# Optimization experiments

Hardware: AMD Instinct MI355X
Metric: run time of the kernel (lower is better)

The kernel has to match this reference:

```python
import jax, jax.numpy as jnp
import numpy as np

T, B, F = 128, 128, 1024
ALPHA_BASE, LAMBDA_BASE = 0.97, 0.95
THETA_BASE, BETA_THETA = 0.1, 0.01
RHO, GATE_ALPHA = 0.25, 5.0        # gate_cfg rho_B/rho_C, alpha
NUDGE, PHASE_SCALE = 0.1, 0.02     # gate_cfg additive_nudge, ei_cfg phase_corr_scale
MIX_AMP, MIX_NOV, MIX_INST = 1.0, 0.5, 0.5


def _adaptive_percentile_threshold(score, rho, alpha):
    # keep top-rho fraction per row: tau = (1-rho)-quantile, soft sigmoid gate
    tau = jnp.quantile(score, 1.0 - rho, axis=-1, keepdims=True)
    return jax.nn.sigmoid(alpha * (score - tau)), tau


def setup_inputs() -> dict:
    key = jax.random.key(0)
    k0, k1, k2, k3 = jax.random.split(key, 4)
    return {
        "in_re": jax.random.normal(k0, (T, B, F), jnp.float32),
        "in_im": jax.random.normal(k1, (T, B, F), jnp.float32),
        "r_re": 0.05 * jax.random.normal(k2, (F,), jnp.float32),
        "r_im": 0.05 * jax.random.normal(k3, (F,), jnp.float32),
        "alpha_map": jnp.zeros((F,), jnp.float32),
        "lambda_map": jnp.zeros((F,), jnp.float32),
    }


def reference(in_re, in_im, r_re, r_im, alpha_map, lambda_map):
    sg = jax.lax.stop_gradient
    alpha = jnp.clip(ALPHA_BASE + 0.05 * jnp.tanh(alpha_map), 0.9, 0.995)  # [F]
    lam = jnp.clip(LAMBDA_BASE + 0.05 * jnp.tanh(lambda_map), 0.9, 0.995)  # [F]
    r_conj = jnp.conj(r_re + 1j * r_im)                                    # [F] c64
    theta_base = jnp.full((F,), THETA_BASE, jnp.float32)
    in_field = (in_re + 1j * in_im).astype(jnp.complex64)                  # [T,B,F]

    carry0 = dict(
        X=jnp.zeros((B, F), jnp.complex64),
        sA=jnp.zeros((B, F), jnp.float32),
        sB=jnp.zeros((B, F), jnp.float32),
        sC=jnp.zeros((B, F), jnp.float32),
        theta=theta_base,
        mu=jnp.zeros((F,), jnp.float32),
        var=jnp.full((F,), 0.01, jnp.float32),
        ema_unit=jnp.zeros((F,), jnp.complex64),
        b_usage=jnp.zeros((F,), jnp.float32),
        c_usage=jnp.zeros((F,), jnp.float32),
    )

    def step(c, u):
        X_mid = alpha * c["X"] + u                       # [B,F] c64
        amp = jnp.abs(X_mid)
        unit = jnp.exp(1j * jnp.angle(X_mid))            # unit phase
        # EMA stats (torch.no_grad -> stop_gradient)
        mu = sg(0.9 * c["mu"] + 0.1 * amp.mean(0))
        var = sg(0.9 * c["var"] + 0.1 * ((amp - mu[None]) ** 2).mean(0))
        ema_unit = sg(0.9 * c["ema_unit"] + 0.1 * unit.mean(0))
        plv = jnp.abs(ema_unit)                          # [F]
        zscore = (amp - mu[None]) / (jnp.sqrt(var)[None] + 1e-3)
        instab = (1.0 - plv)[None]
        score = MIX_AMP * amp + MIX_NOV * jnp.abs(zscore) + MIX_INST * instab
        gB, _ = _adaptive_percentile_threshold(score, RHO, GATE_ALPHA)
        gC, _ = _adaptive_percentile_threshold(-score, RHO, GATE_ALPHA)
        XB = X_mid * gB
        XC = X_mid * gC
        sA = lam * c["sA"] + jnp.real(X_mid * r_conj)
        sB = lam * c["sB"] + jnp.real(XB * r_conj)
        sC = lam * c["sC"] + jnp.real(XC * r_conj)
        evA = (sA >= c["theta"]).astype(jnp.float32)
        evB = (sB >= c["theta"]).astype(jnp.float32)
        evC = (sC >= c["theta"]).astype(jnp.float32)
        # threshold homeostasis (no_grad)
        theta = c["theta"] + 0.01 * evB.mean(0) - 0.01 * evC.mean(0)
        theta = jnp.clip(theta - BETA_THETA * (theta - theta_base), 0.01, 10.0)
        # reentry_mode='full': phase correction + additive nudge
        corr = (evB.mean(0) > 0).astype(jnp.float32)[None]  # [1,F]
        XA = X_mid * jnp.exp(1j * PHASE_SCALE * corr)
        XA = XA + NUDGE * (XB * corr)
        b_usage = 0.99 * c["b_usage"] + 0.01 * evB.mean(0)
        c_usage = 0.99 * c["c_usage"] + 0.01 * evC.mean(0)
        new = dict(X=XA, sA=sA, sB=sB, sC=sC, theta=theta, mu=mu, var=var,
                   ema_unit=ema_unit, b_usage=b_usage, c_usage=c_usage)
        return new, sA

    _, sA_seq = jax.lax.scan(step, carry0, in_field)
    return sA_seq  # [T,B,F]
```

## Files before the change

### kernel.cpp

```cpp
#include <hip/hip_runtime.h>
#include <math.h>


#define T_STEPS 128
#define B_DIM   128
#define F_DIM   1024
#define NWG     128
#define NTH     1024
#define BF      (B_DIM * F_DIM)

typedef unsigned long long ull;

__device__ __forceinline__ ull ld64(const ull* p) {
  return __hip_atomic_load(p, __ATOMIC_RELAXED, __HIP_MEMORY_SCOPE_AGENT);
}
__device__ __forceinline__ void st64(ull* p, ull v) {
  __hip_atomic_store(p, v, __ATOMIC_RELAXED, __HIP_MEMORY_SCOPE_AGENT);
}

extern "C" __global__ void __launch_bounds__(NTH)
ResonatorABC_82094004896068_kernel(
    const float* __restrict__ in_re, const float* __restrict__ in_im,
    const float* __restrict__ r_re_p, const float* __restrict__ r_im_p,
    const float* __restrict__ alpha_map, const float* __restrict__ lambda_map,
    float* __restrict__ out, ull* __restrict__ ws)
{
  const int tid  = threadIdx.x;
  const int wg   = blockIdx.x;
  const int b    = tid >> 3;
  const int fl   = tid & 7;
  const int f    = (wg << 3) + fl;
  const int wid  = tid >> 6;
  const int lane = tid & 63;
  const int idx  = b * F_DIM + f;

  ull* score64 = ws;
  ull* tauB64  = ws + BF;
  ull* tauC64  = ws + BF + 128;

  __shared__ __align__(16) float pamp[16][8][4];
  __shared__ __align__(16) float pfin[8][4];
  __shared__ __align__(16) float pev[16][8][2];
  __shared__ __align__(16) float evfin[8][2];
  __shared__ unsigned h[1024];
  __shared__ unsigned wsum[16];
  __shared__ unsigned mmw[16][2];
  __shared__ unsigned mmu[2];
  __shared__ unsigned tbin[4], tbase[4], tcnt[4];
  __shared__ unsigned lcnt[4];
  __shared__ unsigned lists[4][256];
  __shared__ unsigned resv[4], resf[4];
  __shared__ unsigned rmm[2];
  __shared__ unsigned t2[3];
  __shared__ float tauLds[256];

  float af = fminf(fmaxf(0.97f + 0.05f * tanhf(alpha_map[f]), 0.90f), 0.995f);
  float lf = fminf(fmaxf(0.95f + 0.05f * tanhf(lambda_map[f]), 0.90f), 0.995f);
  float rr = r_re_p[f];
  float ri = r_im_p[f];
  const float c002 = cosf(0.02f);
  const float s002 = sinf(0.02f);

  float X_re = 0.f, X_im = 0.f, sA = 0.f, sB = 0.f, sC = 0.f;
  float mu = 0.f, var = 0.01f, theta = 0.1f, ema_re = 0.f, ema_im = 0.f;

  float ur = in_re[idx];
  float ui = in_im[idx];

  const unsigned KR0 = 255u, KR1 = 256u, KR2 = 767u, KR3 = 768u;

  for (int t = 0; t < T_STEPS; ++t) {
    const ull want = (ull)(t + 1);

    h[tid] = 0u;

    float Xm_re = af * X_re + ur;
    float Xm_im = af * X_im + ui;
    float amp2 = Xm_re * Xm_re + Xm_im * Xm_im;
    float amp  = sqrtf(amp2);
    float invamp = (amp > 0.f) ? (1.0f / amp) : 0.f;
    float un_re = (amp > 0.f) ? (Xm_re * invamp) : 1.0f;
    float un_im = Xm_im * invamp;
    float proj = Xm_re * rr + Xm_im * ri;
    sA = lf * sA + proj;
    out[t * BF + idx] = sA;

    float r0 = amp, r1 = amp2, r2 = un_re, r3 = un_im;
    #pragma unroll
    for (int m = 8; m < 64; m <<= 1) {
      r0 += __shfl_xor(r0, m);
      r1 += __shfl_xor(r1, m);
      r2 += __shfl_xor(r2, m);
      r3 += __shfl_xor(r3, m);
    }
    if (lane < 8) { *(float4*)&pamp[wid][lane][0] = make_float4(r0, r1, r2, r3); }
    __syncthreads();
    if (tid < 32) {
      int sfl = tid >> 2, q = tid & 3;
      float s = 0.f;
      #pragma unroll
      for (int w = 0; w < 16; ++w) s += pamp[w][sfl][q];
      pfin[sfl][q] = s;
    }
    __syncthreads();
    float4 SS = *(const float4*)&pfin[fl][0];
    float m1 = SS.x * 0.0078125f;
    float m2 = SS.y * 0.0078125f;
    mu = 0.9f * mu + 0.1f * m1;
    float vm = m2 - 2.f * mu * m1 + mu * mu;
    vm = fmaxf(vm, 0.f);
    var = 0.9f * var + 0.1f * vm;
    ema_re = 0.9f * ema_re + 0.1f * (SS.z * 0.0078125f);
    ema_im = 0.9f * ema_im + 0.1f * (SS.w * 0.0078125f);
    float plv = sqrtf(ema_re * ema_re + ema_im * ema_im);
    float zs = (amp - mu) / (sqrtf(var) + 1e-3f);
    float score = amp + 0.5f * fabsf(zs) + 0.5f * (1.0f - plv);
    st64(&score64[idx], (want << 32) | (ull)__float_as_uint(score));

    float ur_n = 0.f, ui_n = 0.f;
    if (t + 1 < T_STEPS) {
      ur_n = in_re[(t + 1) * BF + idx];
      ui_n = in_im[(t + 1) * BF + idx];
    }

    const ull* spoll = &score64[wg * F_DIM + tid];
    ull v = ld64(spoll);
    while ((v >> 32) != want) { __builtin_amdgcn_s_sleep(1); v = ld64(spoll); }
    unsigned uval = (unsigned)v;

    unsigned umin = uval, umax = uval;
    #pragma unroll
    for (int m = 1; m < 64; m <<= 1) {
      umin = min(umin, (unsigned)__shfl_xor((int)umin, m));
      umax = max(umax, (unsigned)__shfl_xor((int)umax, m));
    }
    if (lane == 0) { mmw[wid][0] = umin; mmw[wid][1] = umax; }
    __syncthreads();
    if (tid < 16) {
      unsigned a = mmw[tid][0], c = mmw[tid][1];
      #pragma unroll
      for (int m = 1; m < 16; m <<= 1) {
        a = min(a, (unsigned)__shfl_xor((int)a, m));
        c = max(c, (unsigned)__shfl_xor((int)c, m));
      }
      if (tid == 0) { mmu[0] = a; mmu[1] = c; }
    }
    __syncthreads();
    unsigned lo = mmu[0], hi = mmu[1];

    if (lo != hi) {
      ull rng = (ull)hi - (ull)lo + 1ull;
      ull inv = (1ull << 40) / rng;
      unsigned bin = (unsigned)((((ull)(uval - lo)) * inv) >> 30);
      atomicAdd(&h[bin], 1u);
      __syncthreads();
      unsigned cnt = h[tid];
      unsigned incl = cnt;
      #pragma unroll
      for (int d = 1; d < 64; d <<= 1) {
        unsigned vv = __shfl_up(incl, d);
        if (lane >= d) incl += vv;
      }
      if (lane == 63) wsum[wid] = incl;
      __syncthreads();
      if (tid < 16) {
        unsigned wv = wsum[tid], wincl = wv;
        #pragma unroll
        for (int d = 1; d < 16; d <<= 1) {
          unsigned x = __shfl_up(wincl, d);
          if (tid >= d) wincl += x;
        }
        wsum[tid] = wincl - wv;
      }
      if (tid < 4) { lcnt[tid] = 0u; resf[tid] = 0u; }
      __syncthreads();
      unsigned base = wsum[wid] + (incl - cnt);
      if (cnt > 0u) {
        if (base <= KR0 && KR0 < base + cnt) { tbin[0] = tid; tbase[0] = base; tcnt[0] = cnt; }
        if (base <= KR1 && KR1 < base + cnt) { tbin[1] = tid; tbase[1] = base; tcnt[1] = cnt; }
        if (base <= KR2 && KR2 < base + cnt) { tbin[2] = tid; tbase[2] = base; tcnt[2] = cnt; }
        if (base <= KR3 && KR3 < base + cnt) { tbin[3] = tid; tbase[3] = base; tcnt[3] = cnt; }
      }
      __syncthreads();
      unsigned b0 = tbin[0], b1 = tbin[1], b2 = tbin[2], b3 = tbin[3];
      if (bin == b0) { unsigned s = atomicAdd(&lcnt[0], 1u); if (s < 256u) lists[0][s] = uval; }
      else if (bin == b1 && b1 != b0) { unsigned s = atomicAdd(&lcnt[1], 1u); if (s < 256u) lists[1][s] = uval; }
      else if (bin == b2 && b2 != b1) { unsigned s = atomicAdd(&lcnt[2], 1u); if (s < 256u) lists[2][s] = uval; }
      else if (bin == b3 && b3 != b2) { unsigned s = atomicAdd(&lcnt[3], 1u); if (s < 256u) lists[3][s] = uval; }
      __syncthreads();
      if (wid < 4) {
        const int j = wid;
        const unsigned KRj = (j == 0) ? KR0 : (j == 1) ? KR1 : (j == 2) ? KR2 : KR3;
        int src = j;
        while (src > 0 && tbin[src - 1] == tbin[j]) --src;
        unsigned c = tcnt[j];
        if (c <= 256u) {
          unsigned kk = KRj - tbase[j];
          for (int bi = 0; bi < (int)c; bi += 64) {
            int i = bi + lane;
            if (i < (int)c) {
              unsigned e = lists[src][i];
              unsigned r = 0;
              for (int q = 0; q < (int)c; ++q) {
                unsigned x = lists[src][q];
                r += (x < e || (x == e && q < i)) ? 1u : 0u;
              }
              if (r == kk) { resv[j] = e; resf[j] = 1u; }
            }
          }
        }
      }
      __syncthreads();
      for (int j = 0; j < 4; ++j) {
        if (resf[j]) continue;
        const unsigned KRj = (j == 0) ? KR0 : (j == 1) ? KR1 : (j == 2) ? KR2 : KR3;
        bool inj = (bin == tbin[j]);
        unsigned krem = KRj - tbase[j];
        for (int iter = 0; iter < 40; ++iter) {
          if (tid == 0) { rmm[0] = 0xFFFFFFFFu; rmm[1] = 0u; }
          __syncthreads();
          if (inj) { atomicMin(&rmm[0], uval); atomicMax(&rmm[1], uval); }
          __syncthreads();
          unsigned wlo = rmm[0], whi = rmm[1];
          if (wlo == whi) { if (tid == 0) { resv[j] = wlo; resf[j] = 1u; } __syncthreads(); break; }
          h[tid] = 0u;
          __syncthreads();
          ull rng2 = (ull)whi - (ull)wlo + 1ull;
          ull inv2 = (1ull << 40) / rng2;
          unsigned nb = inj ? (unsigned)((((ull)(uval - wlo)) * inv2) >> 30) : 0u;
          if (inj) atomicAdd(&h[nb], 1u);
          __syncthreads();
          unsigned cnt2 = h[tid];
          unsigned incl2 = cnt2;
          #pragma unroll
          for (int d = 1; d < 64; d <<= 1) {
            unsigned vv = __shfl_up(incl2, d);
            if (lane >= d) incl2 += vv;
          }
          if (lane == 63) wsum[wid] = incl2;
          __syncthreads();
          if (tid < 16) {
            unsigned wv = wsum[tid], wincl = wv;
            #pragma unroll
            for (int d = 1; d < 16; d <<= 1) {
              unsigned x = __shfl_up(wincl, d);
              if (tid >= d) wincl += x;
            }
            wsum[tid] = wincl - wv;
          }
          if (tid == 0) lcnt[0] = 0u;
          __syncthreads();
          unsigned base2 = wsum[wid] + (incl2 - cnt2);
          if (cnt2 > 0u && base2 <= krem && krem < base2 + cnt2) {
            t2[0] = tid; t2[1] = base2; t2[2] = cnt2;
          }
          __syncthreads();
          unsigned nbin = t2[0], nbase = t2[1], ncnt = t2[2];
          bool newin = inj && (nb == nbin);
          if (ncnt <= 256u) {
            if (newin) { unsigned s = atomicAdd(&lcnt[0], 1u); if (s < 256u) lists[0][s] = uval; }
            __syncthreads();
            if (wid == 0) {
              unsigned kk2 = krem - nbase;
              for (int bi = 0; bi < (int)ncnt; bi += 64) {
                int i = bi + lane;
                if (i < (int)ncnt) {
                  unsigned e = lists[0][i];
                  unsigned r = 0;
                  for (int q = 0; q < (int)ncnt; ++q) {
                    unsigned x = lists[0][q];
                    r += (x < e || (x == e && q < i)) ? 1u : 0u;
                  }
                  if (r == kk2) { resv[j] = e; resf[j] = 1u; }
                }
              }
            }
            __syncthreads();
            break;
          }
          inj = newin; krem = krem - nbase;
        }
      }
    } else {
      if (tid < 4) { resv[tid] = lo; resf[tid] = 1u; }
      __syncthreads();
    }
    if (tid == 0) {
      float s255 = __uint_as_float(resv[0]);
      float s256 = __uint_as_float(resv[1]);
      float s767 = __uint_as_float(resv[2]);
      float s768 = __uint_as_float(resv[3]);
      float tb = 0.75f * s767 + 0.25f * s768;
      float tc = -(0.75f * s256 + 0.25f * s255);
      st64(&tauB64[wg], (want << 32) | (ull)__float_as_uint(tb));
      st64(&tauC64[wg], (want << 32) | (ull)__float_as_uint(tc));
    }

    if (tid < 256) {
      const ull* src = (tid < 128) ? &tauB64[tid] : &tauC64[tid - 128];
      ull v2 = ld64(src);
      while ((v2 >> 32) != want) { __builtin_amdgcn_s_sleep(1); v2 = ld64(src); }
      tauLds[tid] = __uint_as_float((unsigned)v2);
    }
    __syncthreads();
    float tb = tauLds[b];
    float tc = tauLds[128 + b];

    float gB = 1.0f / (1.0f + expf(-5.0f * (score - tb)));
    float gC = 1.0f / (1.0f + expf(-5.0f * (-score - tc)));
    sB = lf * sB + proj * gB;
    sC = lf * sC + proj * gC;
    float e0 = (sB >= theta) ? 1.0f : 0.0f;
    float e1 = (sC >= theta) ? 1.0f : 0.0f;
    #pragma unroll
    for (int m = 8; m < 64; m <<= 1) {
      e0 += __shfl_xor(e0, m);
      e1 += __shfl_xor(e1, m);
    }
    if (lane < 8) { pev[wid][lane][0] = e0; pev[wid][lane][1] = e1; }
    __syncthreads();
    if (tid < 16) {
      int sfl = tid >> 1, q = tid & 1;
      float s = 0.f;
      #pragma unroll
      for (int w = 0; w < 16; ++w) s += pev[w][sfl][q];
      evfin[sfl][q] = s;
    }
    __syncthreads();
    float cB = evfin[fl][0];
    float cC = evfin[fl][1];
    float th1 = theta + 0.01f * (cB * 0.0078125f) - 0.01f * (cC * 0.0078125f);
    theta = fminf(fmaxf(th1 - 0.01f * (th1 - 0.1f), 0.01f), 10.0f);
    float fac_re = 1.0f, fac_im = 0.0f;
    if (cB > 0.f) { fac_re = c002 + 0.1f * gB; fac_im = s002; }
    X_re = Xm_re * fac_re - Xm_im * fac_im;
    X_im = Xm_re * fac_im + Xm_im * fac_re;

    ur = ur_n; ui = ui_n;
  }
}

extern "C" void kernel_launch(void* const* d_in, const int* in_sizes, int n_in,
                              void* d_out, int out_size, void* d_ws, size_t ws_size,
                              hipStream_t stream) {
  const float* in_re = (const float*)d_in[0];
  const float* in_im = (const float*)d_in[1];
  const float* r_re  = (const float*)d_in[2];
  const float* r_im  = (const float*)d_in[3];
  const float* amap  = (const float*)d_in[4];
  const float* lmap  = (const float*)d_in[5];
  float* out = (float*)d_out;
  ull* ws = (ull*)d_ws;
  hipMemsetAsync(d_ws, 0, (size_t)(BF + 256) * 8, stream);
  hipLaunchKernelGGL(ResonatorABC_82094004896068_kernel,
                     dim3(NWG), dim3(NTH), 0, stream,
                     in_re, in_im, r_re, r_im, amap, lmap, out, ws);
}
```

Measured before the change: 1.255 ms.

## Shrink workgroup to 256 threads, each handling four batch rows

Cuts the workgroup from 1024 threads to 256, with each thread handling four batch rows (b = rg + 32k) for the same feature column. Histogram, scan, min/max and event reductions are restructured to work on four elements per thread, with 4-wave cross-wave combines replacing 16-wave ones and one barrier round dropped. The aim is lower barrier and cross-wave reduction cost in this latency-bound, barrier-heavy per-timestep loop. The trade-off is more serial work per thread and more registers, which may lengthen the per-step critical path.

After: 1.208 ms. 1.04x faster.

```diff
diff --git a/kernel.cpp b/kernel.cpp
--- a/kernel.cpp
+++ b/kernel.cpp
@@ -6,7 +6,7 @@
 #define B_DIM   128
 #define F_DIM   1024
 #define NWG     128
-#define NTH     1024
+#define NTH     256
 #define BF      (B_DIM * F_DIM)
 
 typedef unsigned long long ull;
@@ -27,25 +27,23 @@
 {
   const int tid  = threadIdx.x;
   const int wg   = blockIdx.x;
-  const int b    = tid >> 3;
   const int fl   = tid & 7;
+  const int rg   = tid >> 3;
   const int f    = (wg << 3) + fl;
   const int wid  = tid >> 6;
   const int lane = tid & 63;
-  const int idx  = b * F_DIM + f;
 
   ull* score64 = ws;
   ull* tauB64  = ws + BF;
   ull* tauC64  = ws + BF + 128;
 
-  __shared__ __align__(16) float pamp[16][8][4];
+  __shared__ __align__(16) float pamp[4][8][4];
   __shared__ __align__(16) float pfin[8][4];
-  __shared__ __align__(16) float pev[16][8][2];
+  __shared__ __align__(16) float pev[4][8][2];
   __shared__ __align__(16) float evfin[8][2];
-  __shared__ unsigned h[1024];
-  __shared__ unsigned wsum[16];
-  __shared__ unsigned mmw[16][2];
-  __shared__ unsigned mmu[2];
+  __shared__ __align__(16) unsigned h[1024];
+  __shared__ unsigned wsum[4];
+  __shared__ unsigned mmw[4][2];
   __shared__ unsigned tbin[4], tbase[4], tcnt[4];
   __shared__ unsigned lcnt[4];
   __shared__ unsigned lists[4][256];
@@ -54,53 +52,61 @@
   __shared__ unsigned t2[3];
   __shared__ float tauLds[256];
 
-  float af = fminf(fmaxf(0.97f + 0.05f * tanhf(alpha_map[f]), 0.90f), 0.995f);
-  float lf = fminf(fmaxf(0.95f + 0.05f * tanhf(lambda_map[f]), 0.90f), 0.995f);
-  float rr = r_re_p[f];
-  float ri = r_im_p[f];
+  const float af = fminf(fmaxf(0.97f + 0.05f * tanhf(alpha_map[f]), 0.90f), 0.995f);
+  const float lf = fminf(fmaxf(0.95f + 0.05f * tanhf(lambda_map[f]), 0.90f), 0.995f);
+  const float rr = r_re_p[f];
+  const float ri = r_im_p[f];
   const float c002 = cosf(0.02f);
   const float s002 = sinf(0.02f);
 
-  float X_re = 0.f, X_im = 0.f, sA = 0.f, sB = 0.f, sC = 0.f;
+  float X_re[4] = {0.f,0.f,0.f,0.f}, X_im[4] = {0.f,0.f,0.f,0.f};
+  float sA[4] = {0.f,0.f,0.f,0.f}, sB[4] = {0.f,0.f,0.f,0.f}, sC[4] = {0.f,0.f,0.f,0.f};
   float mu = 0.f, var = 0.01f, theta = 0.1f, ema_re = 0.f, ema_im = 0.f;
 
-  float ur = in_re[idx];
-  float ui = in_im[idx];
-
-  const unsigned KR0 = 255u, KR1 = 256u, KR2 = 767u, KR3 = 768u;
+  int idx[4];
+  float ur[4], ui[4];
+  #pragma unroll
+  for (int k = 0; k < 4; ++k) {
+    idx[k] = (rg + 32 * k) * F_DIM + f;
+    ur[k] = in_re[idx[k]];
+    ui[k] = in_im[idx[k]];
+  }
+
+  const unsigned KR[4] = {255u, 256u, 767u, 768u};
 
   for (int t = 0; t < T_STEPS; ++t) {
     const ull want = (ull)(t + 1);
 
-    h[tid] = 0u;
-
-    float Xm_re = af * X_re + ur;
-    float Xm_im = af * X_im + ui;
-    float amp2 = Xm_re * Xm_re + Xm_im * Xm_im;
-    float amp  = sqrtf(amp2);
-    float invamp = (amp > 0.f) ? (1.0f / amp) : 0.f;
-    float un_re = (amp > 0.f) ? (Xm_re * invamp) : 1.0f;
-    float un_im = Xm_im * invamp;
-    float proj = Xm_re * rr + Xm_im * ri;
-    sA = lf * sA + proj;
-    out[t * BF + idx] = sA;
-
-    float r0 = amp, r1 = amp2, r2 = un_re, r3 = un_im;
+    *(uint4*)&h[4 * tid] = make_uint4(0u, 0u, 0u, 0u);
+
+    float Xm_re[4], Xm_im[4], proj[4], amp[4], score[4];
+    float a0 = 0.f, a1 = 0.f, a2 = 0.f, a3 = 0.f;
+    #pragma unroll
+    for (int k = 0; k < 4; ++k) {
+      Xm_re[k] = af * X_re[k] + ur[k];
+      Xm_im[k] = af * X_im[k] + ui[k];
+      float amp2 = Xm_re[k] * Xm_re[k] + Xm_im[k] * Xm_im[k];
+      amp[k] = sqrtf(amp2);
+      float invamp = (amp[k] > 0.f) ? (1.0f / amp[k]) : 0.f;
+      float un_re = (amp[k] > 0.f) ? (Xm_re[k] * invamp) : 1.0f;
+      float un_im = Xm_im[k] * invamp;
+      proj[k] = Xm_re[k] * rr + Xm_im[k] * ri;
+      sA[k] = lf * sA[k] + proj[k];
+      out[t * BF + idx[k]] = sA[k];
+      a0 += amp[k]; a1 += amp2; a2 += un_re; a3 += un_im;
+    }
     #pragma unroll
     for (int m = 8; m < 64; m <<= 1) {
-      r0 += __shfl_xor(r0, m);
-      r1 += __shfl_xor(r1, m);
-      r2 += __shfl_xor(r2, m);
-      r3 += __shfl_xor(r3, m);
-    }
-    if (lane < 8) { *(float4*)&pamp[wid][lane][0] = make_float4(r0, r1, r2, r3); }
+      a0 += __shfl_xor(a0, m);
+      a1 += __shfl_xor(a1, m);
+      a2 += __shfl_xor(a2, m);
+      a3 += __shfl_xor(a3, m);
+    }
+    if (lane < 8) { *(float4*)&pamp[wid][lane][0] = make_float4(a0, a1, a2, a3); }
     __syncthreads();
     if (tid < 32) {
       int sfl = tid >> 2, q = tid & 3;
-      float s = 0.f;
-      #pragma unroll
-      for (int w = 0; w < 16; ++w) s += pamp[w][sfl][q];
-      pfin[sfl][q] = s;
+      pfin[sfl][q] = pamp[0][sfl][q] + pamp[1][sfl][q] + pamp[2][sfl][q] + pamp[3][sfl][q];
     }
     __syncthreads();
     float4 SS = *(const float4*)&pfin[fl][0];
@@ -113,22 +119,35 @@
     ema_re = 0.9f * ema_re + 0.1f * (SS.z * 0.0078125f);
     ema_im = 0.9f * ema_im + 0.1f * (SS.w * 0.0078125f);
     float plv = sqrtf(ema_re * ema_re + ema_im * ema_im);
-    float zs = (amp - mu) / (sqrtf(var) + 1e-3f);
-    float score = amp + 0.5f * fabsf(zs) + 0.5f * (1.0f - plv);
-    st64(&score64[idx], (want << 32) | (ull)__float_as_uint(score));
-
-    float ur_n = 0.f, ui_n = 0.f;
+    float sden = sqrtf(var) + 1e-3f;
+    #pragma unroll
+    for (int k = 0; k < 4; ++k) {
+      float zs = (amp[k] - mu) / sden;
+      score[k] = amp[k] + 0.5f * fabsf(zs) + 0.5f * (1.0f - plv);
+      st64(&score64[idx[k]], (want << 32) | (ull)__float_as_uint(score[k]));
+    }
+
+    float ur_n[4] = {0.f,0.f,0.f,0.f}, ui_n[4] = {0.f,0.f,0.f,0.f};
     if (t + 1 < T_STEPS) {
-      ur_n = in_re[(t + 1) * BF + idx];
-      ui_n = in_im[(t + 1) * BF + idx];
-    }
-
-    const ull* spoll = &score64[wg * F_DIM + tid];
-    ull v = ld64(spoll);
-    while ((v >> 32) != want) { __builtin_amdgcn_s_sleep(1); v = ld64(spoll); }
-    unsigned uval = (unsigned)v;
-
-    unsigned umin = uval, umax = uval;
+      #pragma unroll
+      for (int k = 0; k < 4; ++k) {
+        ur_n[k] = in_re[(t + 1) * BF + idx[k]];
+        ui_n[k] = in_im[(t + 1) * BF + idx[k]];
+      }
+    }
+
+    unsigned uval[4], bin[4];
+    {
+      const ull* sp0 = &score64[wg * F_DIM + tid];
+      #pragma unroll
+      for (int k = 0; k < 4; ++k) {
+        ull v = ld64(sp0 + 256 * k);
+        while ((v >> 32) != want) { __builtin_amdgcn_s_sleep(1); v = ld64(sp0 + 256 * k); }
+        uval[k] = (unsigned)v;
+      }
+    }
+    unsigned umin = min(min(uval[0], uval[1]), min(uval[2], uval[3]));
+    unsigned umax = max(max(uval[0], uval[1]), max(uval[2], uval[3]));
     #pragma unroll
     for (int m = 1; m < 64; m <<= 1) {
       umin = min(umin, (unsigned)__shfl_xor((int)umin, m));
@@ -136,26 +155,22 @@
     }
     if (lane == 0) { mmw[wid][0] = umin; mmw[wid][1] = umax; }
     __syncthreads();
-    if (tid < 16) {
-      unsigned a = mmw[tid][0], c = mmw[tid][1];
-      #pragma unroll
-      for (int m = 1; m < 16; m <<= 1) {
-        a = min(a, (unsigned)__shfl_xor((int)a, m));
-        c = max(c, (unsigned)__shfl_xor((int)c, m));
-      }
-      if (tid == 0) { mmu[0] = a; mmu[1] = c; }
-    }
-    __syncthreads();
-    unsigned lo = mmu[0], hi = mmu[1];
+    unsigned lo = min(min(mmw[0][0], mmw[1][0]), min(mmw[2][0], mmw[3][0]));
+    unsigned hi = max(max(mmw[0][1], mmw[1][1]), max(mmw[2][1], mmw[3][1]));
 
     if (lo != hi) {
       ull rng = (ull)hi - (ull)lo + 1ull;
       ull inv = (1ull << 40) / rng;
-      unsigned bin = (unsigned)((((ull)(uval - lo)) * inv) >> 30);
-      atomicAdd(&h[bin], 1u);
-      __syncthreads();
-      unsigned cnt = h[tid];
-      unsigned incl = cnt;
+      #pragma unroll
+      for (int k = 0; k < 4; ++k) {
+        bin[k] = (unsigned)((((ull)(uval[k] - lo)) * inv) >> 30);
+        atomicAdd(&h[bin[k]], 1u);
+      }
+      if (tid < 4) { lcnt[tid] = 0u; resf[tid] = 0u; }
+      __syncthreads();
+      uint4 hc = *(const uint4*)&h[4 * tid];
+      unsigned s4 = hc.x + hc.y + hc.z + hc.w;
+      unsigned incl = s4;
       #pragma unroll
       for (int d = 1; d < 64; d <<= 1) {
         unsigned vv = __shfl_up(incl, d);
@@ -163,39 +178,41 @@
       }
       if (lane == 63) wsum[wid] = incl;
       __syncthreads();
-      if (tid < 16) {
-        unsigned wv = wsum[tid], wincl = wv;
-        #pragma unroll
-        for (int d = 1; d < 16; d <<= 1) {
-          unsigned x = __shfl_up(wincl, d);
-          if (tid >= d) wincl += x;
+      unsigned woff = 0u;
+      for (int w = 0; w < 4; ++w) if (w < wid) woff += wsum[w];
+      unsigned gexcl = woff + incl - s4;
+      unsigned cv[4] = {hc.x, hc.y, hc.z, hc.w};
+      unsigned bb[4];
+      bb[0] = gexcl; bb[1] = bb[0] + cv[0]; bb[2] = bb[1] + cv[1]; bb[3] = bb[2] + cv[2];
+      #pragma unroll
+      for (int i = 0; i < 4; ++i) {
+        if (cv[i] > 0u) {
+          #pragma unroll
+          for (int r = 0; r < 4; ++r) {
+            if (bb[i] <= KR[r] && KR[r] < bb[i] + cv[i]) {
+              tbin[r] = 4 * tid + i; tbase[r] = bb[i]; tcnt[r] = cv[i];
+            }
+          }
         }
-        wsum[tid] = wincl - wv;
-      }
-      if (tid < 4) { lcnt[tid] = 0u; resf[tid] = 0u; }
-      __syncthreads();
-      unsigned base = wsum[wid] + (incl - cnt);
-      if (cnt > 0u) {
-        if (base <= KR0 && KR0 < base + cnt) { tbin[0] = tid; tbase[0] = base; tcnt[0] = cnt; }
-        if (base <= KR1 && KR1 < base + cnt) { tbin[1] = tid; tbase[1] = base; tcnt[1] = cnt; }
-        if (base <= KR2 && KR2 < base + cnt) { tbin[2] = tid; tbase[2] = base; tcnt[2] = cnt; }
-        if (base <= KR3 && KR3 < base + cnt) { tbin[3] = tid; tbase[3] = base; tcnt[3] = cnt; }
       }
       __syncthreads();
       unsigned b0 = tbin[0], b1 = tbin[1], b2 = tbin[2], b3 = tbin[3];
-      if (bin == b0) { unsigned s = atomicAdd(&lcnt[0], 1u); if (s < 256u) lists[0][s] = uval; }
-      else if (bin == b1 && b1 != b0) { unsigned s = atomicAdd(&lcnt[1], 1u); if (s < 256u) lists[1][s] = uval; }
-      else if (bin == b2 && b2 != b1) { unsigned s = atomicAdd(&lcnt[2], 1u); if (s < 256u) lists[2][s] = uval; }
-      else if (bin == b3 && b3 != b2) { unsigned s = atomicAdd(&lcnt[3], 1u); if (s < 256u) lists[3][s] = uval; }
-      __syncthreads();
-      if (wid < 4) {
+      #pragma unroll
+      for (int k = 0; k < 4; ++k) {
+        unsigned bk = bin[k], uv = uval[k];
+        if (bk == b0) { unsigned s = atomicAdd(&lcnt[0], 1u); if (s < 256u) lists[0][s] = uv; }
+        else if (bk == b1 && b1 != b0) { unsigned s = atomicAdd(&lcnt[1], 1u); if (s < 256u) lists[1][s] = uv; }
+        else if (bk == b2 && b2 != b1) { unsigned s = atomicAdd(&lcnt[2], 1u); if (s < 256u) lists[2][s] = uv; }
+        else if (bk == b3 && b3 != b2) { unsigned s = atomicAdd(&lcnt[3], 1u); if (s < 256u) lists[3][s] = uv; }
+      }
+      __syncthreads();
+      {
         const int j = wid;
-        const unsigned KRj = (j == 0) ? KR0 : (j == 1) ? KR1 : (j == 2) ? KR2 : KR3;
         int src = j;
         while (src > 0 && tbin[src - 1] == tbin[j]) --src;
         unsigned c = tcnt[j];
         if (c <= 256u) {
-          unsigned kk = KRj - tbase[j];
+          unsigned kk = KR[j] - tbase[j];
           for (int bi = 0; bi < (int)c; bi += 64) {
             int i = bi + lane;
             if (i < (int)c) {
@@ -213,52 +230,62 @@
       __syncthreads();
       for (int j = 0; j < 4; ++j) {
         if (resf[j]) continue;
-        const unsigned KRj = (j == 0) ? KR0 : (j == 1) ? KR1 : (j == 2) ? KR2 : KR3;
-        bool inj = (bin == tbin[j]);
-        unsigned krem = KRj - tbase[j];
+        bool inj[4];
+        #pragma unroll
+        for (int k = 0; k < 4; ++k) inj[k] = (bin[k] == tbin[j]);
+        unsigned krem = KR[j] - tbase[j];
         for (int iter = 0; iter < 40; ++iter) {
           if (tid == 0) { rmm[0] = 0xFFFFFFFFu; rmm[1] = 0u; }
           __syncthreads();
-          if (inj) { atomicMin(&rmm[0], uval); atomicMax(&rmm[1], uval); }
+          #pragma unroll
+          for (int k = 0; k < 4; ++k)
+            if (inj[k]) { atomicMin(&rmm[0], uval[k]); atomicMax(&rmm[1], uval[k]); }
           __syncthreads();
           unsigned wlo = rmm[0], whi = rmm[1];
           if (wlo == whi) { if (tid == 0) { resv[j] = wlo; resf[j] = 1u; } __syncthreads(); break; }
-          h[tid] = 0u;
+          *(uint4*)&h[4 * tid] = make_uint4(0u, 0u, 0u, 0u);
           __syncthreads();
           ull rng2 = (ull)whi - (ull)wlo + 1ull;
           ull inv2 = (1ull << 40) / rng2;
-          unsigned nb = inj ? (unsigned)((((ull)(uval - wlo)) * inv2) >> 30) : 0u;
-          if (inj) atomicAdd(&h[nb], 1u);
-          __syncthreads();
-          unsigned cnt2 = h[tid];
-          unsigned incl2 = cnt2;
+          unsigned nb[4];
+          #pragma unroll
+          for (int k = 0; k < 4; ++k) {
+            nb[k] = inj[k] ? (unsigned)((((ull)(uval[k] - wlo)) * inv2) >> 30) : 0u;
+            if (inj[k]) atomicAdd(&h[nb[k]], 1u);
+          }
+          __syncthreads();
+          uint4 hc2 = *(const uint4*)&h[4 * tid];
+          unsigned s42 = hc2.x + hc2.y + hc2.z + hc2.w;
+          unsigned incl2 = s42;
           #pragma unroll
           for (int d = 1; d < 64; d <<= 1) {
             unsigned vv = __shfl_up(incl2, d);
             if (lane >= d) incl2 += vv;
           }
           if (lane == 63) wsum[wid] = incl2;
-          __syncthreads();
-          if (tid < 16) {
-            unsigned wv = wsum[tid], wincl = wv;
+          if (tid == 0) lcnt[0] = 0u;
+          __syncthreads();
+          unsigned woff2 = 0u;
+          for (int w = 0; w < 4; ++w) if (w < wid) woff2 += wsum[w];
+          unsigned gexcl2 = woff2 + incl2 - s42;
+          unsigned cv2[4] = {hc2.x, hc2.y, hc2.z, hc2.w};
+          unsigned bb2[4];
+          bb2[0] = gexcl2; bb2[1] = bb2[0] + cv2[0]; bb2[2] = bb2[1] + cv2[1]; bb2[3] = bb2[2] + cv2[2];
+          #pragma unroll
+          for (int i = 0; i < 4; ++i) {
+            if (cv2[i] > 0u && bb2[i] <= krem && krem < bb2[i] + cv2[i]) {
+              t2[0] = 4 * tid + i; t2[1] = bb2[i]; t2[2] = cv2[i];
+            }
+          }
+          __syncthreads();
+          unsigned nbin = t2[0], nbase = t2[1], ncnt = t2[2];
+          bool newin[4];
+          #pragma unroll
+          for (int k = 0; k < 4; ++k) newin[k] = inj[k] && (nb[k] == nbin);
+          if (ncnt <= 256u) {
             #pragma unroll
-            for (int d = 1; d < 16; d <<= 1) {
-              unsigned x = __shfl_up(wincl, d);
-              if (tid >= d) wincl += x;
-            }
-            wsum[tid] = wincl - wv;
-          }
-          if (tid == 0) lcnt[0] = 0u;
-          __syncthreads();
-          unsigned base2 = wsum[wid] + (incl2 - cnt2);
-          if (cnt2 > 0u && base2 <= krem && krem < base2 + cnt2) {
-            t2[0] = tid; t2[1] = base2; t2[2] = cnt2;
-          }
-          __syncthreads();
-          unsigned nbin = t2[0], nbase = t2[1], ncnt = t2[2];
-          bool newin = inj && (nb == nbin);
-          if (ncnt <= 256u) {
-            if (newin) { unsigned s = atomicAdd(&lcnt[0], 1u); if (s < 256u) lists[0][s] = uval; }
+            for (int k = 0; k < 4; ++k)
+              if (newin[k]) { unsigned s = atomicAdd(&lcnt[0], 1u); if (s < 256u) lists[0][s] = uval[k]; }
             __syncthreads();
             if (wid == 0) {
               unsigned kk2 = krem - nbase;
@@ -278,7 +305,9 @@
             __syncthreads();
             break;
           }
-          inj = newin; krem = krem - nbase;
+          #pragma unroll
+          for (int k = 0; k < 4; ++k) inj[k] = newin[k];
+          krem -= nbase;
         }
       }
     } else {
@@ -296,22 +325,28 @@
       st64(&tauC64[wg], (want << 32) | (ull)__float_as_uint(tc));
     }
 
-    if (tid < 256) {
+    {
       const ull* src = (tid < 128) ? &tauB64[tid] : &tauC64[tid - 128];
       ull v2 = ld64(src);
       while ((v2 >> 32) != want) { __builtin_amdgcn_s_sleep(1); v2 = ld64(src); }
       tauLds[tid] = __uint_as_float((unsigned)v2);
     }
     __syncthreads();
-    float tb = tauLds[b];
-    float tc = tauLds[128 + b];
-
-    float gB = 1.0f / (1.0f + expf(-5.0f * (score - tb)));
-    float gC = 1.0f / (1.0f + expf(-5.0f * (-score - tc)));
-    sB = lf * sB + proj * gB;
-    sC = lf * sC + proj * gC;
-    float e0 = (sB >= theta) ? 1.0f : 0.0f;
-    float e1 = (sC >= theta) ? 1.0f : 0.0f;
+
+    float gB[4];
+    float e0 = 0.f, e1 = 0.f;
+    #pragma unroll
+    for (int k = 0; k < 4; ++k) {
+      float tb = tauLds[rg + 32 * k];
+      float tc = tauLds[128 + rg + 32 * k];
+      float sc = score[k];
+      gB[k] = 1.0f / (1.0f + expf(-5.0f * (sc - tb)));
+      float gC = 1.0f / (1.0f + expf(-5.0f * (-sc - tc)));
+      sB[k] = lf * sB[k] + proj[k] * gB[k];
+      sC[k] = lf * sC[k] + proj[k] * gC;
+      e0 += (sB[k] >= theta) ? 1.0f : 0.0f;
+      e1 += (sC[k] >= theta) ? 1.0f : 0.0f;
+    }
     #pragma unroll
     for (int m = 8; m < 64; m <<= 1) {
       e0 += __shfl_xor(e0, m);
@@ -321,22 +356,22 @@
     __syncthreads();
     if (tid < 16) {
       int sfl = tid >> 1, q = tid & 1;
-      float s = 0.f;
-      #pragma unroll
-      for (int w = 0; w < 16; ++w) s += pev[w][sfl][q];
-      evfin[sfl][q] = s;
+      evfin[sfl][q] = pev[0][sfl][q] + pev[1][sfl][q] + pev[2][sfl][q] + pev[3][sfl][q];
     }
     __syncthreads();
     float cB = evfin[fl][0];
     float cC = evfin[fl][1];
     float th1 = theta + 0.01f * (cB * 0.0078125f) - 0.01f * (cC * 0.0078125f);
     theta = fminf(fmaxf(th1 - 0.01f * (th1 - 0.1f), 0.01f), 10.0f);
-    float fac_re = 1.0f, fac_im = 0.0f;
-    if (cB > 0.f) { fac_re = c002 + 0.1f * gB; fac_im = s002; }
-    X_re = Xm_re * fac_re - Xm_im * fac_im;
-    X_im = Xm_re * fac_im + Xm_im * fac_re;
-
-    ur = ur_n; ui = ui_n;
+    bool corr = (cB > 0.f);
+    #pragma unroll
+    for (int k = 0; k < 4; ++k) {
+      float fac_re = corr ? (c002 + 0.1f * gB[k]) : 1.0f;
+      float fac_im = corr ? s002 : 0.0f;
+      X_re[k] = Xm_re[k] * fac_re - Xm_im[k] * fac_im;
+      X_im[k] = Xm_re[k] * fac_im + Xm_im[k] * fac_re;
+      ur[k] = ur_n[k]; ui[k] = ui_n[k];
+    }
   }
 }
 
```
